# Kernel optimization log

Hardware: AMD Instinct MI355X
Metric: run time of the kernel (lower is better)

The kernel has to match this reference:

```python
import jax, jax.numpy as jnp
import numpy as np

# norse default LIFParameters
DT = 1e-3
TAU_SYN_INV = 200.0
TAU_MEM_INV = 100.0
V_LEAK = 0.0
V_TH = 1.0
V_RESET = 0.0


def heaviside(x):
    return (x > 0).astype(x.dtype)


def setup_inputs() -> dict:
    key = jax.random.key(0)
    ks = jax.random.split(key, 5)
    T, B, I, H, O = 14, 4096, 2048, 1024, 128
    x = (jax.random.uniform(ks[0], (T, B, I), dtype=jnp.float32) < 0.2).astype(jnp.float32)  # spike train
    w_in = jax.random.normal(ks[1], (H, I), dtype=jnp.float32) * (1.0 / np.sqrt(I))
    w_rec = jax.random.normal(ks[2], (H, H), dtype=jnp.float32) * (1.0 / np.sqrt(H))
    out_w = jax.random.normal(ks[3], (O, H), dtype=jnp.float32) * (1.0 / np.sqrt(H))
    out_b = jax.random.normal(ks[4], (O,), dtype=jnp.float32) * 0.01
    return {"x": x, "w_in": w_in, "w_rec": w_rec, "out_w": out_w, "out_b": out_b}


def reference(x, w_in, w_rec, out_w, out_b):
    T, B, _ = x.shape
    H = w_in.shape[0]
    z0 = jnp.zeros((B, H), dtype=x.dtype)
    v0 = jnp.full((B, H), V_LEAK, dtype=x.dtype)
    i0 = jnp.zeros((B, H), dtype=x.dtype)

    def step(carry, x_t):
        z, v, i = carry
        v_dec = v + DT * TAU_MEM_INV * ((V_LEAK - v) + i)   # membrane integration
        i_dec = i - DT * TAU_SYN_INV * i                    # synaptic decay
        z_new = heaviside(v_dec - V_TH)                     # spike
        v_new = (1.0 - z_new) * v_dec + z_new * V_RESET     # reset
        i_new = i_dec + x_t @ w_in.T + z @ w_rec.T          # input + recurrent current
        return (z_new, v_new, i_new), None

    (z_T, _, _), _ = jax.lax.scan(step, (z0, v0, i0), x)
    return z_T @ out_w.T + out_b
```

## Files before the change

kernel.cpp:

```cpp
#include <hip/hip_runtime.h>
#include <stdint.h>

#define T_STEPS 14
#define B_DIM   4096
#define I_DIM   2048
#define H_DIM   1024
#define O_DIM   128
#define K_TOT   3072

#define WSCALE_F 33554432.0f

typedef __bf16  bf16x8  __attribute__((ext_vector_type(8)));
typedef float   floatx4 __attribute__((ext_vector_type(4)));
typedef int     int4v   __attribute__((ext_vector_type(4)));
typedef int     int16v  __attribute__((ext_vector_type(16)));

__device__ __forceinline__ uint16_t f2bf_rne(float f) {
    uint32_t u = __float_as_uint(f);
    u += 0x7fffu + ((u >> 16) & 1u);
    return (uint16_t)(u >> 16);
}
__device__ __forceinline__ float bf2f(uint16_t h) {
    return __uint_as_float(((uint32_t)h) << 16);
}

__device__ __forceinline__ void gload_lds16(const void* g, void* l) {
    __builtin_amdgcn_global_load_lds((__attribute__((address_space(1))) void*)g,
                                     (__attribute__((address_space(3))) void*)l, 16, 0, 0);
}


__global__ void split_w_kernel(const float* __restrict__ w_in, const float* __restrict__ w_rec,
                               int8_t* __restrict__ WB) {
    int idx = blockIdx.x * 256 + threadIdx.x;
    int h = idx / K_TOT;
    int k = idx - h * K_TOT;
    float w = (k < I_DIM) ? w_in[(size_t)h * I_DIM + k]
                          : w_rec[(size_t)h * H_DIM + (k - I_DIM)];
    int W  = __float2int_rn(w * WSCALE_F);
    int d0 = (int8_t)(W & 0xFF);
    int r1 = (W - d0) >> 8;
    int d1 = (int8_t)(r1 & 0xFF);
    int d2 = (r1 - d1) >> 8;
    int nt = h >> 5, n32 = h & 31;
    int ktw = k >> 7, k128 = k & 127;
    int kk = k128 >> 5, half = (k128 >> 4) & 1, j = k128 & 15;
    int lane = half * 32 + n32;
    size_t base = (size_t)(nt * 24 + ktw) * 12288 + kk * 1024 + lane * 16 + j;
    WB[base] = (int8_t)d0; WB[base + 4096] = (int8_t)d1; WB[base + 8192] = (int8_t)d2;
}

__global__ void split_ow_kernel(const float* __restrict__ out_w, uint16_t* __restrict__ OW3) {
    int idx = blockIdx.x * 256 + threadIdx.x;
    float w = out_w[idx];
    uint16_t hi = f2bf_rne(w);
    float r1 = w - bf2f(hi);
    uint16_t mid = f2bf_rne(r1);
    float r2 = r1 - bf2f(mid);
    uint16_t lo = f2bf_rne(r2);
    const size_t S = (size_t)O_DIM * H_DIM;
    OW3[idx] = hi; OW3[idx + S] = mid; OW3[idx + 2 * S] = lo;
}

__global__ void cvt_x_kernel(const float* __restrict__ x, int8_t* __restrict__ xb) {
    size_t gid = (size_t)blockIdx.x * 256 + threadIdx.x;
    int g = (int)(gid & 1023);
    size_t chunk = gid >> 10;
    int kt   = (int)(chunk & 15);
    int mIdx = (int)((chunk >> 4) & 31);
    int t    = (int)(chunk >> 9);
    int group = g >> 8, kk = (g >> 6) & 3, lane = g & 63;
    int half = lane >> 5, row32 = lane & 31;
    int b = mIdx * 128 + group * 32 + row32;
    int k = kt * 128 + kk * 32 + half * 16;
    const float4* src = (const float4*)(x + ((size_t)t * B_DIM + b) * I_DIM + k);
    union { int8_t bytes[16]; int4v v; } u;
#pragma unroll
    for (int q = 0; q < 4; ++q) {
        float4 f = src[q];
        u.bytes[q * 4 + 0] = (int8_t)(f.x > 0.5f);
        u.bytes[q * 4 + 1] = (int8_t)(f.y > 0.5f);
        u.bytes[q * 4 + 2] = (int8_t)(f.z > 0.5f);
        u.bytes[q * 4 + 3] = (int8_t)(f.w > 0.5f);
    }
    ((int4v*)xb)[gid] = u.v;
}

__launch_bounds__(256, 4)
__global__ void lif_step_kernel(const int8_t* __restrict__ Xt,
                                const int8_t* __restrict__ Zin,
                                const int8_t* __restrict__ WB,
                                float2* __restrict__ VI,
                                int8_t* __restrict__ Zout,
                                uint16_t* __restrict__ Zbf, int t) {
    __shared__ int8_t sA[16384];
    __shared__ int8_t sB[12288];

    const int tid  = threadIdx.x;
    const int wave = tid >> 6, lane = tid & 63;
    const int lane32 = lane & 31, hl = lane >> 5;

    const int nt = blockIdx.x & 31, mIdx = blockIdx.x >> 5;
    const int mBase = mIdx * 128, nBase = nt * 32;

    int16v acc[3] = {};

    const int nIters = (t > 0) ? 24 : 16;

    for (int kt = 0; kt < nIters; ++kt) {
        __syncthreads();
        const int8_t* chunkA = (kt < 16)
            ? Xt  + ((size_t)mIdx * 16 + kt) * 16384
            : Zin + ((size_t)mIdx * 8 + (kt - 16)) * 16384;
#pragma unroll
        for (int j = 0; j < 4; ++j) {
            const int seg = j * 4 + wave;
            gload_lds16(chunkA + seg * 1024 + lane * 16, &sA[seg * 1024]);
        }
        const int8_t* chunkB = WB + (size_t)(nt * 24 + kt) * 12288;
#pragma unroll
        for (int j = 0; j < 3; ++j) {
            const int seg = j * 4 + wave;
            gload_lds16(chunkB + seg * 1024 + lane * 16, &sB[seg * 1024]);
        }
        __syncthreads();
#pragma unroll
        for (int kk = 0; kk < 4; ++kk) {
            int4v aF = *(const int4v*)&sA[wave * 4096 + kk * 1024 + lane * 16];
#pragma unroll
            for (int s = 0; s < 3; ++s) {
                int4v bF = *(const int4v*)&sB[s * 4096 + kk * 1024 + lane * 16];
                acc[s] = __builtin_amdgcn_mfma_i32_32x32x32_i8(aF, bF, acc[s], 0, 0, 0);
            }
        }
    }

    int8_t* zchunk = Zout + ((size_t)mIdx * 8 + (nt >> 2)) * 16384;
#pragma unroll
    for (int r = 0; r < 16; ++r) {
#pragma clang fp contract(off)
        float cur = (float)acc[2][r] * (1.0f / 512.0f)
                  + (float)acc[1][r] * (1.0f / 131072.0f)
                  + (float)acc[0][r] * (1.0f / 33554432.0f);
        int row = (r & 3) + 8 * (r >> 2) + 4 * hl;
        int b = mBase + wave * 32 + row;
        int h = nBase + lane32;
        size_t idx = (size_t)b * H_DIM + h;
        float v, ii;
        if (t == 0) { v = 0.0f; ii = 0.0f; }
        else        { float2 vi = VI[idx]; v = vi.x; ii = vi.y; }
        float v_dec = v + 0.1f * ((0.0f - v) + ii);
        float i_dec = ii - 0.2f * ii;
        bool z = (v_dec > 1.0f);
        float2 vi_new;
        vi_new.x = z ? 0.0f : v_dec;
        vi_new.y = i_dec + cur;
        VI[idx] = vi_new;
        if (t == T_STEPS - 1) {
            Zbf[idx] = z ? (uint16_t)0x3F80 : (uint16_t)0;
        } else {
            zchunk[wave * 4096 + (nt & 3) * 1024
                   + ((lane32 >> 4) * 32 + row) * 16 + (lane32 & 15)]
                = z ? (int8_t)1 : (int8_t)0;
        }
    }
}

__launch_bounds__(256)
__global__ void out_gemm_kernel(const uint16_t* __restrict__ Zfin,
                                const uint16_t* __restrict__ OW3,
                                const float* __restrict__ out_b,
                                float* __restrict__ out) {
    __shared__ uint16_t sA[128 * 32];
    __shared__ uint16_t sB[3][128 * 32];

    const int tid  = threadIdx.x;
    const int wave = tid >> 6, lane = tid & 63;
    const int wm = wave >> 1, wn = wave & 1;
    const int quad = lane >> 4, col = lane & 15;

    const int mBase = blockIdx.x * 128;

    floatx4 acc[4][4] = {};

    const int sRowA = wave * 16 + (lane >> 2);
    const int sCol  = (lane & 3) * 8;

    for (int kt = 0; kt < H_DIM / 32; ++kt) {
        const int kb = kt * 32;
        __syncthreads();
#pragma unroll
        for (int j = 0; j < 2; ++j) {
            const uint16_t* g = Zfin + (size_t)(mBase + j * 64 + sRowA) * H_DIM + kb + sCol;
            gload_lds16(g, &sA[(j * 64 + wave * 16) * 32]);
        }
#pragma unroll
        for (int s = 0; s < 3; ++s) {
            const uint16_t* wsrc = OW3 + (size_t)s * O_DIM * H_DIM;
#pragma unroll
            for (int j = 0; j < 2; ++j) {
                const uint16_t* g = wsrc + (size_t)(j * 64 + sRowA) * H_DIM + kb + sCol;
                gload_lds16(g, &sB[s][(j * 64 + wave * 16) * 32]);
            }
        }
        __syncthreads();

        bf16x8 aF[4];
#pragma unroll
        for (int mi = 0; mi < 4; ++mi) {
            int row = wm * 64 + mi * 16 + col;
            aF[mi] = *reinterpret_cast<const bf16x8*>(&sA[row * 32 + quad * 8]);
        }
#pragma unroll
        for (int s = 0; s < 3; ++s) {
            bf16x8 bF[4];
#pragma unroll
            for (int ni = 0; ni < 4; ++ni) {
                int row = wn * 64 + ni * 16 + col;
                bF[ni] = *reinterpret_cast<const bf16x8*>(&sB[s][row * 32 + quad * 8]);
            }
#pragma unroll
            for (int mi = 0; mi < 4; ++mi)
#pragma unroll
                for (int ni = 0; ni < 4; ++ni)
                    acc[mi][ni] = __builtin_amdgcn_mfma_f32_16x16x32_bf16(
                        aF[mi], bF[ni], acc[mi][ni], 0, 0, 0);
        }
    }

    {
#pragma clang fp contract(off)
#pragma unroll
        for (int mi = 0; mi < 4; ++mi)
#pragma unroll
            for (int ni = 0; ni < 4; ++ni)
#pragma unroll
                for (int r = 0; r < 4; ++r) {
                    int b = mBase + wm * 64 + mi * 16 + quad * 4 + r;
                    int h = wn * 64 + ni * 16 + col;
                    out[(size_t)b * O_DIM + h] = acc[mi][ni][r] + out_b[h];
                }
    }
}

extern "C" void kernel_launch(void* const* d_in, const int* in_sizes, int n_in,
                              void* d_out, int out_size, void* d_ws, size_t ws_size,
                              hipStream_t stream) {
    const float* x     = (const float*)d_in[0];
    const float* w_in  = (const float*)d_in[1];
    const float* w_rec = (const float*)d_in[2];
    const float* out_w = (const float*)d_in[3];
    const float* out_b = (const float*)d_in[4];
    float* out = (float*)d_out;

    char* ws = (char*)d_ws;
    size_t off = 0;
    int8_t*   WB   = (int8_t*)(ws + off);   off += (size_t)3 * H_DIM * K_TOT;
    uint16_t* OW3  = (uint16_t*)(ws + off); off += (size_t)3 * O_DIM * H_DIM * 2;
    int8_t*   Xall = (int8_t*)(ws + off);   off += (size_t)T_STEPS * B_DIM * I_DIM;
    uint16_t* Zbf  = (uint16_t*)(ws + off); off += (size_t)B_DIM * H_DIM * 2;
    int8_t*   Z0   = (int8_t*)(ws + off);   off += (size_t)B_DIM * H_DIM;
    int8_t*   Z1   = (int8_t*)(ws + off);   off += (size_t)B_DIM * H_DIM;
    float2*   VI   = (float2*)(ws + off);   off += (size_t)B_DIM * H_DIM * 8;

    split_w_kernel<<<(H_DIM * K_TOT) / 256, 256, 0, stream>>>(w_in, w_rec, WB);
    split_ow_kernel<<<(O_DIM * H_DIM) / 256, 256, 0, stream>>>(out_w, OW3);
    cvt_x_kernel<<<(int)(((size_t)T_STEPS * B_DIM * I_DIM / 16) / 256), 256, 0, stream>>>(x, Xall);

    int8_t* zbuf[2] = { Z0, Z1 };
    for (int t = 0; t < T_STEPS; ++t) {
        lif_step_kernel<<<dim3(1024), 256, 0, stream>>>(
            Xall + (size_t)t * 32 * 16 * 16384, zbuf[t & 1], WB, VI,
            zbuf[(t + 1) & 1], Zbf, t);
    }
    out_gemm_kernel<<<B_DIM / 128, 256, 0, stream>>>(Zbf, OW3, out_b, out);
}
```

Baseline: 1.373 ms.

## Double M tile per block in LIF step kernel to reuse weight fragments

Each block now covers 256 batch rows instead of 128, and each wave computes two 32-row M tiles against the same three B fragments. Every weight tile loaded into LDS is reused for twice as many rows, which halves weight traffic and LDS B reads per MFMA. In exchange the grid shrinks to 512 blocks, LDS use grows, the occupancy hint drops to 2 blocks per CU, and the accumulators double, which may cost latency hiding.

```diff
diff --git a/kernel.cpp b/kernel.cpp
--- a/kernel.cpp
+++ b/kernel.cpp
@@ -67,11 +67,11 @@
     int g = (int)(gid & 1023);
     size_t chunk = gid >> 10;
     int kt   = (int)(chunk & 15);
-    int mIdx = (int)((chunk >> 4) & 31);
+    int mc   = (int)((chunk >> 4) & 31);
     int t    = (int)(chunk >> 9);
     int group = g >> 8, kk = (g >> 6) & 3, lane = g & 63;
     int half = lane >> 5, row32 = lane & 31;
-    int b = mIdx * 128 + group * 32 + row32;
+    int b = mc * 128 + group * 32 + row32;
     int k = kt * 128 + kk * 32 + half * 16;
     const float4* src = (const float4*)(x + ((size_t)t * B_DIM + b) * I_DIM + k);
     union { int8_t bytes[16]; int4v v; } u;
@@ -86,14 +86,14 @@
     ((int4v*)xb)[gid] = u.v;
 }
 
-__launch_bounds__(256, 4)
+__launch_bounds__(256, 2)
 __global__ void lif_step_kernel(const int8_t* __restrict__ Xt,
                                 const int8_t* __restrict__ Zin,
                                 const int8_t* __restrict__ WB,
                                 float2* __restrict__ VI,
                                 int8_t* __restrict__ Zout,
                                 uint16_t* __restrict__ Zbf, int t) {
-    __shared__ int8_t sA[16384];
+    __shared__ int8_t sA[32768];
     __shared__ int8_t sB[12288];
 
     const int tid  = threadIdx.x;
@@ -101,22 +101,25 @@
     const int lane32 = lane & 31, hl = lane >> 5;
 
     const int nt = blockIdx.x & 31, mIdx = blockIdx.x >> 5;
-    const int mBase = mIdx * 128, nBase = nt * 32;
-
-    int16v acc[3] = {};
+    const int mBase = mIdx * 256, nBase = nt * 32;
+
+    const int chunkIdx = 2 * mIdx + (wave >> 1);
+    const int halfSel  = wave & 1;
+
+    int16v acc[2][3] = {};
 
     const int nIters = (t > 0) ? 24 : 16;
 
     for (int kt = 0; kt < nIters; ++kt) {
         __syncthreads();
         const int8_t* chunkA = (kt < 16)
-            ? Xt  + ((size_t)mIdx * 16 + kt) * 16384
-            : Zin + ((size_t)mIdx * 8 + (kt - 16)) * 16384;
-#pragma unroll
-        for (int j = 0; j < 4; ++j) {
-            const int seg = j * 4 + wave;
-            gload_lds16(chunkA + seg * 1024 + lane * 16, &sA[seg * 1024]);
-        }
+            ? Xt  + ((size_t)chunkIdx * 16 + kt) * 16384
+            : Zin + ((size_t)chunkIdx * 8 + (kt - 16)) * 16384;
+        const int8_t* srcA = chunkA + halfSel * 8192;
+        int8_t* dstA = &sA[wave * 8192];
+#pragma unroll
+        for (int j = 0; j < 8; ++j)
+            gload_lds16(srcA + j * 1024 + lane * 16, dstA + j * 1024);
         const int8_t* chunkB = WB + (size_t)(nt * 24 + kt) * 12288;
 #pragma unroll
         for (int j = 0; j < 3; ++j) {
@@ -126,44 +129,48 @@
         __syncthreads();
 #pragma unroll
         for (int kk = 0; kk < 4; ++kk) {
-            int4v aF = *(const int4v*)&sA[wave * 4096 + kk * 1024 + lane * 16];
+            int4v a0 = *(const int4v*)&sA[wave * 8192 + kk * 1024 + lane * 16];
+            int4v a1 = *(const int4v*)&sA[wave * 8192 + 4096 + kk * 1024 + lane * 16];
 #pragma unroll
             for (int s = 0; s < 3; ++s) {
                 int4v bF = *(const int4v*)&sB[s * 4096 + kk * 1024 + lane * 16];
-                acc[s] = __builtin_amdgcn_mfma_i32_32x32x32_i8(aF, bF, acc[s], 0, 0, 0);
-            }
-        }
-    }
-
-    int8_t* zchunk = Zout + ((size_t)mIdx * 8 + (nt >> 2)) * 16384;
-#pragma unroll
-    for (int r = 0; r < 16; ++r) {
+                acc[0][s] = __builtin_amdgcn_mfma_i32_32x32x32_i8(a0, bF, acc[0][s], 0, 0, 0);
+                acc[1][s] = __builtin_amdgcn_mfma_i32_32x32x32_i8(a1, bF, acc[1][s], 0, 0, 0);
+            }
+        }
+    }
+
+    int8_t* zchunk = Zout + ((size_t)chunkIdx * 8 + (nt >> 2)) * 16384;
+#pragma unroll
+    for (int mi = 0; mi < 2; ++mi)
+#pragma unroll
+        for (int r = 0; r < 16; ++r) {
 #pragma clang fp contract(off)
-        float cur = (float)acc[2][r] * (1.0f / 512.0f)
-                  + (float)acc[1][r] * (1.0f / 131072.0f)
-                  + (float)acc[0][r] * (1.0f / 33554432.0f);
-        int row = (r & 3) + 8 * (r >> 2) + 4 * hl;
-        int b = mBase + wave * 32 + row;
-        int h = nBase + lane32;
-        size_t idx = (size_t)b * H_DIM + h;
-        float v, ii;
-        if (t == 0) { v = 0.0f; ii = 0.0f; }
-        else        { float2 vi = VI[idx]; v = vi.x; ii = vi.y; }
-        float v_dec = v + 0.1f * ((0.0f - v) + ii);
-        float i_dec = ii - 0.2f * ii;
-        bool z = (v_dec > 1.0f);
-        float2 vi_new;
-        vi_new.x = z ? 0.0f : v_dec;
-        vi_new.y = i_dec + cur;
-        VI[idx] = vi_new;
-        if (t == T_STEPS - 1) {
-            Zbf[idx] = z ? (uint16_t)0x3F80 : (uint16_t)0;
-        } else {
-            zchunk[wave * 4096 + (nt & 3) * 1024
-                   + ((lane32 >> 4) * 32 + row) * 16 + (lane32 & 15)]
-                = z ? (int8_t)1 : (int8_t)0;
-        }
-    }
+            float cur = (float)acc[mi][2][r] * (1.0f / 512.0f)
+                      + (float)acc[mi][1][r] * (1.0f / 131072.0f)
+                      + (float)acc[mi][0][r] * (1.0f / 33554432.0f);
+            int row = (r & 3) + 8 * (r >> 2) + 4 * hl;
+            int b = mBase + wave * 64 + mi * 32 + row;
+            int h = nBase + lane32;
+            size_t idx = (size_t)b * H_DIM + h;
+            float v, ii;
+            if (t == 0) { v = 0.0f; ii = 0.0f; }
+            else        { float2 vi = VI[idx]; v = vi.x; ii = vi.y; }
+            float v_dec = v + 0.1f * ((0.0f - v) + ii);
+            float i_dec = ii - 0.2f * ii;
+            bool z = (v_dec > 1.0f);
+            float2 vi_new;
+            vi_new.x = z ? 0.0f : v_dec;
+            vi_new.y = i_dec + cur;
+            VI[idx] = vi_new;
+            if (t == T_STEPS - 1) {
+                Zbf[idx] = z ? (uint16_t)0x3F80 : (uint16_t)0;
+            } else {
+                zchunk[(halfSel * 2 + mi) * 4096 + (nt & 3) * 1024
+                       + ((lane32 >> 4) * 32 + row) * 16 + (lane32 & 15)]
+                    = z ? (int8_t)1 : (int8_t)0;
+            }
+        }
 }
 
 __launch_bounds__(256)
@@ -269,7 +276,7 @@
 
     int8_t* zbuf[2] = { Z0, Z1 };
     for (int t = 0; t < T_STEPS; ++t) {
-        lif_step_kernel<<<dim3(1024), 256, 0, stream>>>(
+        lif_step_kernel<<<dim3(512), 256, 0, stream>>>(
             Xall + (size_t)t * 32 * 16 * 16384, zbuf[t & 1], WB, VI,
             zbuf[(t + 1) & 1], Zbf, t);
     }
```

Measured after the change: 1.377 ms. Within noise of the previous version (+0.3%).
